# Optimization experiments

Hardware: AMD Instinct MI355X
Metric: run time of the kernel (lower is better)

Reference implementation:

```python
import jax, jax.numpy as jnp
import numpy as np

DIM_MODEL = 1024
DIM_LLM = 4096
HEAD_NUM = 16
DIM_KEYS = DIM_MODEL // HEAD_NUM  # 64


def setup_inputs() -> dict:
    key = jax.random.key(0)
    ks = jax.random.split(key, 11)
    B, P, V = 8, 256, 8192
    s_q = 1.0 / np.sqrt(DIM_MODEL)
    s_l = 1.0 / np.sqrt(DIM_LLM)
    s_d = 1.0 / np.sqrt(DIM_MODEL)
    return {
        "query": jax.random.normal(ks[0], (B, P, DIM_MODEL), dtype=jnp.float32),
        "key": jax.random.normal(ks[1], (V, DIM_LLM), dtype=jnp.float32),
        "value": jax.random.normal(ks[2], (V, DIM_LLM), dtype=jnp.float32),
        "Wq": jax.random.normal(ks[3], (DIM_MODEL, DIM_MODEL), dtype=jnp.float32) * s_q,
        "bq": jnp.zeros((DIM_MODEL,), dtype=jnp.float32),
        "Wk": jax.random.normal(ks[4], (DIM_LLM, DIM_MODEL), dtype=jnp.float32) * s_l,
        "bk": jnp.zeros((DIM_MODEL,), dtype=jnp.float32),
        "Wv": jax.random.normal(ks[5], (DIM_LLM, DIM_MODEL), dtype=jnp.float32) * s_l,
        "bv": jnp.zeros((DIM_MODEL,), dtype=jnp.float32),
        "Wo": jax.random.normal(ks[6], (DIM_MODEL, DIM_LLM), dtype=jnp.float32) * s_d,
        "bo": jnp.zeros((DIM_LLM,), dtype=jnp.float32),
    }


def reference(query, key, value, Wq, bq, Wk, bk, Wv, bv, Wo, bo):
    B, P, _ = query.shape
    V = key.shape[0]
    # projections
    q = (query @ Wq + bq).reshape(B, P, HEAD_NUM, DIM_KEYS)        # [b,p,h,k]
    k = (key @ Wk + bk).reshape(V, HEAD_NUM, DIM_KEYS)             # [v,h,k]
    v = (value @ Wv + bv).reshape(V, HEAD_NUM, DIM_KEYS)           # [v,h,k]
    scale = 1.0 / DIM_KEYS  # NOTE: original uses 1/d_k, not 1/sqrt(d_k)
    scores = jnp.einsum('bphk,vhk->bhpv', q, k)                    # [b,h,p,v]
    A = jax.nn.softmax(scale * scores, axis=-1)                    # dropout is identity in eval
    mapped = jnp.einsum('bhpv,vhk->bphk', A, v)                    # [b,p,h,k]
    mapped = mapped.reshape(B, P, HEAD_NUM * DIM_KEYS)
    return mapped @ Wo + bo                                        # [b,p,dim_llm]
```

## Files before the change

kernel.cpp:

```cpp
#include <hip/hip_runtime.h>


typedef __attribute__((ext_vector_type(8)))  short          short8;
typedef __attribute__((ext_vector_type(4)))  float          f32x4;
typedef __attribute__((ext_vector_type(16))) float          f32x16;
typedef __attribute__((ext_vector_type(8)))  unsigned short ushort8;
typedef __attribute__((ext_vector_type(4)))  unsigned int   uint4v;

__device__ __forceinline__ unsigned short f2bf(float f) {
    unsigned int u = __builtin_bit_cast(unsigned int, f);
    u += 0x7fffu + ((u >> 16) & 1u);
    return (unsigned short)(u >> 16);
}

__device__ __forceinline__ void gld_lds16(const ushort* g, ushort* l) {
    __builtin_amdgcn_global_load_lds(
        (const __attribute__((address_space(1))) void*)g,
        (__attribute__((address_space(3))) void*)l, 16, 0, 0);
}

__global__ __launch_bounds__(256) void conv_f32_bf16(
    const float* __restrict__ in, ushort* __restrict__ out, int n)
{
    int i = (blockIdx.x * 256 + threadIdx.x) * 8;
    if (i >= n) return;
    float4 a = *(const float4*)(in + i);
    float4 b = *(const float4*)(in + i + 4);
    ushort8 o = {f2bf(a.x), f2bf(a.y), f2bf(a.z), f2bf(a.w),
                 f2bf(b.x), f2bf(b.y), f2bf(b.z), f2bf(b.w)};
    *(ushort8*)(out + i) = o;
}

__global__ __launch_bounds__(256) void transconv(
    const float* __restrict__ in, ushort* __restrict__ out, int R, int C)
{
    __shared__ float t[32][33];
    const int tx = threadIdx.x & 31, ty = threadIdx.x >> 5;
    const int bx = blockIdx.x, by = blockIdx.y;
#pragma unroll
    for (int i = 0; i < 4; ++i)
        t[ty + 8 * i][tx] = in[(size_t)(by * 32 + ty + 8 * i) * C + bx * 32 + tx];
    __syncthreads();
#pragma unroll
    for (int i = 0; i < 4; ++i)
        out[(size_t)(bx * 32 + ty + 8 * i) * R + by * 32 + tx] = f2bf(t[tx][ty + 8 * i]);
}

template<int OUT_BF16, int BIAS_ROW>
__global__ __launch_bounds__(256, 4) void gemm_bt(
    const ushort* __restrict__ A, const ushort* __restrict__ BT,
    const float* __restrict__ bias, void* __restrict__ Cout,
    int M, int N, int K, float oscale)
{
    __shared__ ushort As[128 * 32];
    __shared__ ushort Bs[64 * 32];
    const int tid = threadIdx.x;
    const int w = tid >> 6, lane = tid & 63;
    const int m = lane & 15, quad = lane >> 4;
    const int wr = w >> 1, wc = w & 1;
    const int bx = blockIdx.x, by = blockIdx.y;

    f32x4 acc[4][2];
#pragma unroll
    for (int i = 0; i < 4; ++i)
#pragma unroll
        for (int j = 0; j < 2; ++j)
#pragma unroll
            for (int r = 0; r < 4; ++r) acc[i][j][r] = 0.f;

    const int r_i = lane >> 2;
    const int ccl = (lane & 3) ^ ((lane >> 2) & 3) ^ quad;
    const ushort* Ag = A  + (size_t)(by * 128 + w * 32 + r_i) * K + ccl * 8;
    const ushort* Bg = BT + (size_t)(bx * 64 + w * 16 + r_i) * K + ccl * 8;
    ushort* AsW = As + w * 1024;
    ushort* BsW = Bs + w * 512;
    const size_t rowstep = (size_t)16 * K;

    const int phys = (quad ^ (m & 3) ^ (m >> 2)) * 8;
    int aoff[4], boff[2];
#pragma unroll
    for (int i = 0; i < 4; ++i)
        aoff[i] = (wr * 64 + i * 16 + m) * 32 + phys;
#pragma unroll
    for (int j = 0; j < 2; ++j)
        boff[j] = (wc * 32 + j * 16 + m) * 32 + phys;

    const int kIters = K >> 5;
    for (int kt = 0; kt < kIters; ++kt) {
        __syncthreads();
        gld_lds16(Ag, AsW);
        gld_lds16(Ag + rowstep, AsW + 512);
        gld_lds16(Bg, BsW);
        Ag += 32; Bg += 32;
        __syncthreads();
        short8 af[4], bf[2];
#pragma unroll
        for (int i = 0; i < 4; ++i) af[i] = *(const short8*)(As + aoff[i]);
#pragma unroll
        for (int j = 0; j < 2; ++j) bf[j] = *(const short8*)(Bs + boff[j]);
#pragma unroll
        for (int i = 0; i < 4; ++i)
#pragma unroll
            for (int j = 0; j < 2; ++j)
                acc[i][j] = __builtin_amdgcn_mfma_f32_16x16x32_bf16(
                    af[i], bf[j], acc[i][j], 0, 0, 0);
    }

    const int row0 = by * 128 + wr * 64;
    const int col0 = bx * 64 + wc * 32;
#pragma unroll
    for (int i = 0; i < 4; ++i) {
#pragma unroll
        for (int j = 0; j < 2; ++j) {
            const int c = col0 + j * 16 + m;
            float bcol = BIAS_ROW ? 0.f : bias[c];
#pragma unroll
            for (int r = 0; r < 4; ++r) {
                const int rw = row0 + i * 16 + quad * 4 + r;
                float v = acc[i][j][r] + (BIAS_ROW ? bias[rw] : bcol);
                v *= oscale;
                if (OUT_BF16)
                    ((ushort*)Cout)[(size_t)rw * N + c] = f2bf(v);
                else
                    ((float*)Cout)[(size_t)rw * N + c] = v;
            }
        }
    }
}

__global__ __launch_bounds__(512, 4) void attn_mfma(
    const ushort* __restrict__ qb, const ushort* __restrict__ kb,
    const ushort* __restrict__ vT, ushort* __restrict__ mappedb)
{
    __shared__ ushort Qs[64 * 64];
    __shared__ ushort Ks[2][128 * 64];
    __shared__ ushort Vs[2][64 * 128];

    const int tid = threadIdx.x;
    const int w = tid >> 6, lane = tid & 63;
    const int l31 = lane & 31, l5 = lane >> 5, quad = lane >> 4;
    const int wp = w >> 2, wv = w & 3;
    const int idx = blockIdx.x;
    const int pt = idx & 3, h = (idx >> 2) & 15, b = idx >> 6;
    const int pbase = b * 256 + pt * 64;

    const int c8 = lane & 7, r8 = lane >> 3, c16 = lane & 15;
    const int ccK = c8 ^ r8;

    const int t0 = w * 2, t1 = w * 2 + 1;
    const ushort* gk0 = kb + (size_t)(t0 * 8 + r8) * 1024 + h * 64 + ccK * 8;
    const ushort* gk1 = kb + (size_t)(t1 * 8 + r8) * 1024 + h * 64 + ccK * 8;
    const int d0 = t0 * 4 + quad, d1 = t1 * 4 + quad;
    const ushort* gv0 = vT + (size_t)(h * 64 + d0) * 8192 + ((c16 ^ (d0 & 15)) * 8);
    const ushort* gv1 = vT + (size_t)(h * 64 + d1) * 8192 + ((c16 ^ (d1 & 15)) * 8);

    {
        const ushort* g = qb + (size_t)(pbase + w * 8 + r8) * 1024 + h * 64 + c8 * 8;
        gld_lds16(g, Qs + w * 512);
    }
    gld_lds16(gk0, Ks[0] + t0 * 512);
    gld_lds16(gk1, Ks[0] + t1 * 512);
    gld_lds16(gv0, Vs[0] + t0 * 512);
    gld_lds16(gv1, Vs[0] + t1 * 512);
    asm volatile("s_waitcnt vmcnt(4)" ::: "memory");
    __builtin_amdgcn_s_barrier();
    __builtin_amdgcn_sched_barrier(0);
    short8 qf[4];
#pragma unroll
    for (int ks = 0; ks < 4; ++ks)
        qf[ks] = *(const short8*)(Qs + (wp * 32 + l31) * 64 + ks * 16 + l5 * 8);

    f32x16 o[2];
#pragma unroll
    for (int dt = 0; dt < 2; ++dt)
#pragma unroll
        for (int r = 0; r < 16; ++r) o[dt][r] = 0.f;
    float lpart = 0.f;

    for (int t = 0; t < 64; ++t) {
        const int cur = t & 1;
        {
            const size_t koff = (size_t)(((t + 1) & 63) * 128) * 1024;
            const size_t voff = (size_t)(((t + 1) & 63) * 128);
            ushort* KsN = Ks[cur ^ 1];
            ushort* VsN = Vs[cur ^ 1];
            gld_lds16(gk0 + koff, KsN + t0 * 512);
            gld_lds16(gk1 + koff, KsN + t1 * 512);
            gld_lds16(gv0 + voff, VsN + t0 * 512);
            gld_lds16(gv1 + voff, VsN + t1 * 512);
        }
        asm volatile("s_waitcnt vmcnt(4)" ::: "memory");
        __builtin_amdgcn_s_barrier();
        __builtin_amdgcn_sched_barrier(0);

        const ushort* KsC = Ks[cur];
        const ushort* VsC = Vs[cur];

        f32x16 st;
#pragma unroll
        for (int r = 0; r < 16; ++r) st[r] = 0.f;
        {
            const int row = (wv * 32 + l31) * 64;
            const int sw = l31 & 7;
            __builtin_amdgcn_s_setprio(1);
#pragma unroll
            for (int ks = 0; ks < 4; ++ks) {
                const int ph = ((ks * 2 + l5) ^ sw) * 8;
                short8 kf = *(const short8*)(KsC + row + ph);
                st = __builtin_amdgcn_mfma_f32_32x32x16_bf16(kf, qf[ks], st, 0, 0, 0);
            }
            __builtin_amdgcn_s_setprio(0);
        }

#pragma unroll
        for (int k4 = 0; k4 < 2; ++k4) {
            float e[8];
#pragma unroll
            for (int tt = 0; tt < 8; ++tt)
                e[tt] = __builtin_amdgcn_exp2f(st[k4 * 8 + tt]);
            lpart += ((e[0] + e[1]) + (e[2] + e[3])) + ((e[4] + e[5]) + (e[6] + e[7]));
            unsigned int a0, a1, b0, b1;
            asm("v_cvt_pk_bf16_f32 %0, %1, %2" : "=v"(a0) : "v"(e[0]), "v"(e[1]));
            asm("v_cvt_pk_bf16_f32 %0, %1, %2" : "=v"(a1) : "v"(e[2]), "v"(e[3]));
            asm("v_cvt_pk_bf16_f32 %0, %1, %2" : "=v"(b0) : "v"(e[4]), "v"(e[5]));
            asm("v_cvt_pk_bf16_f32 %0, %1, %2" : "=v"(b1) : "v"(e[6]), "v"(e[7]));
            asm("v_permlane32_swap_b32 %0, %1" : "+v"(a0), "+v"(b0));
            asm("v_permlane32_swap_b32 %0, %1" : "+v"(a1), "+v"(b1));
            uint4v pfw = {a0, a1, b0, b1};
            short8 pf = __builtin_bit_cast(short8, pfw);
            const int k8 = wv * 2 + k4;
            __builtin_amdgcn_s_setprio(1);
#pragma unroll
            for (int dt = 0; dt < 2; ++dt) {
                const int d_l = dt * 32 + l31;
                const int ph = ((k8 * 2 + l5) ^ (d_l & 15)) * 8;
                short8 vf = *(const short8*)(VsC + d_l * 128 + ph);
                o[dt] = __builtin_amdgcn_mfma_f32_32x32x16_bf16(pf, vf, o[dt], 0, 0, 0);
            }
            __builtin_amdgcn_s_setprio(0);
        }
        __builtin_amdgcn_sched_barrier(0);
        __builtin_amdgcn_s_barrier();
    }

    float* RedA = (float*)Ks[0];
    float* RedB = (float*)Vs[0];
    float* Lq   = (float*)Qs;
    Lq[w * 64 + lane] = lpart;
    __syncthreads();
    if (wv >= 2) {
        float* R = (wv == 2) ? RedA : RedB;
#pragma unroll
        for (int dt = 0; dt < 2; ++dt)
#pragma unroll
            for (int r = 0; r < 16; ++r)
                R[wp * 2048 + (dt * 16 + r) * 64 + lane] = o[dt][r];
    }
    __syncthreads();
    if (wv < 2) {
        float* R = (wv == 0) ? RedA : RedB;
#pragma unroll
        for (int dt = 0; dt < 2; ++dt)
#pragma unroll
            for (int r = 0; r < 16; ++r)
                o[dt][r] += R[wp * 2048 + (dt * 16 + r) * 64 + lane];
    }
    __syncthreads();
    if (wv == 1) {
#pragma unroll
        for (int dt = 0; dt < 2; ++dt)
#pragma unroll
            for (int r = 0; r < 16; ++r)
                RedA[wp * 2048 + (dt * 16 + r) * 64 + lane] = o[dt][r];
    }
    __syncthreads();
    if (wv == 0) {
#pragma unroll
        for (int dt = 0; dt < 2; ++dt)
#pragma unroll
            for (int r = 0; r < 16; ++r)
                o[dt][r] += RedA[wp * 2048 + (dt * 16 + r) * 64 + lane];
        float lsum = (Lq[(wp * 4 + 0) * 64 + lane] + Lq[(wp * 4 + 1) * 64 + lane])
                   + (Lq[(wp * 4 + 2) * 64 + lane] + Lq[(wp * 4 + 3) * 64 + lane]);

        float lfull = lsum + __shfl_xor(lsum, 32, 64);
        float rinv = 1.0f / lfull;
#pragma unroll
        for (int r = 0; r < 16; ++r) {
            const int poff = (r & 3) + 8 * (r >> 2) + 4 * l5;
            const float sc = __shfl(rinv, poff, 64);
            const size_t grow = (size_t)(pbase + wp * 32 + poff) * 1024;
#pragma unroll
            for (int dt = 0; dt < 2; ++dt)
                mappedb[grow + h * 64 + dt * 32 + l31] = f2bf(o[dt][r] * sc);
        }
    }
}

extern "C" void kernel_launch(void* const* d_in, const int* in_sizes, int n_in,
                              void* d_out, int out_size, void* d_ws, size_t ws_size,
                              hipStream_t stream)
{
    const float* query = (const float*)d_in[0];
    const float* key   = (const float*)d_in[1];
    const float* value = (const float*)d_in[2];
    const float* Wq    = (const float*)d_in[3];
    const float* bq    = (const float*)d_in[4];
    const float* Wk    = (const float*)d_in[5];
    const float* bk    = (const float*)d_in[6];
    const float* Wv    = (const float*)d_in[7];
    const float* bv    = (const float*)d_in[8];
    const float* Wo    = (const float*)d_in[9];
    const float* bo    = (const float*)d_in[10];
    float* out = (float*)d_out;

    char* ws = (char*)d_ws;
    ushort* tmpb    = (ushort*)ws;
    ushort* wslot   = (ushort*)(ws + (64ull << 20));
    ushort* queryb  = (ushort*)(ws + (72ull << 20));
    ushort* qb      = (ushort*)(ws + (76ull << 20));
    ushort* mappedb = (ushort*)ws;
    ushort* kb      = (ushort*)d_out;
    ushort* vT      = (ushort*)((char*)d_out + (16ull << 20));

    const float QSCALE = 1.4426950408889634f / 64.0f;

    conv_f32_bf16<<<16384, 256, 0, stream>>>(key, tmpb, 8192 * 4096);
    transconv<<<dim3(32, 128), 256, 0, stream>>>(Wk, wslot, 4096, 1024);
    gemm_bt<1, 0><<<dim3(16, 64), 256, 0, stream>>>(tmpb, wslot, bk, kb,
                                                    8192, 1024, 4096, 1.0f);
    conv_f32_bf16<<<16384, 256, 0, stream>>>(value, tmpb, 8192 * 4096);
    transconv<<<dim3(32, 128), 256, 0, stream>>>(Wv, wslot, 4096, 1024);
    gemm_bt<1, 1><<<dim3(128, 8), 256, 0, stream>>>(wslot, tmpb, bv, vT,
                                                    1024, 8192, 4096, 1.0f);
    conv_f32_bf16<<<1024, 256, 0, stream>>>(query, queryb, 2048 * 1024);
    transconv<<<dim3(32, 32), 256, 0, stream>>>(Wq, wslot, 1024, 1024);
    gemm_bt<1, 0><<<dim3(16, 16), 256, 0, stream>>>(queryb, wslot, bq, qb,
                                                    2048, 1024, 1024, QSCALE);
    attn_mfma<<<512, 512, 0, stream>>>(qb, kb, vT, mappedb);
    transconv<<<dim3(128, 32), 256, 0, stream>>>(Wo, wslot, 1024, 4096);
    gemm_bt<0, 0><<<dim3(64, 16), 256, 0, stream>>>(mappedb, wslot, bo, out,
                                                    2048, 4096, 1024, 1.0f);
}
```

Baseline: 691.9 us.

## Double-buffer LDS tiles with K=64 stages in bf16 GEMM

The bf16 MFMA GEMM now uses two LDS buffers with a K-tile of 64 instead of one buffer with K=32. The next tile is prefetched via global_load_lds while MFMAs run on the current tile, and the per-iteration barrier count drops from two to one. The XOR swizzle is reworked for 64-element rows. This raises LDS use to 48KB per block and lowers the occupancy hint from 4 to 3 blocks. The last iteration issues a redundant wraparound prefetch, and the mask `& (nk-1)` is only valid when nk is a power of two.

```diff
diff --git a/kernel.cpp b/kernel.cpp
--- a/kernel.cpp
+++ b/kernel.cpp
@@ -47,13 +47,13 @@
 }
 
 template<int OUT_BF16, int BIAS_ROW>
-__global__ __launch_bounds__(256, 4) void gemm_bt(
+__global__ __launch_bounds__(256, 3) void gemm_bt(
     const ushort* __restrict__ A, const ushort* __restrict__ BT,
     const float* __restrict__ bias, void* __restrict__ Cout,
     int M, int N, int K, float oscale)
 {
-    __shared__ ushort As[128 * 32];
-    __shared__ ushort Bs[64 * 32];
+    __shared__ ushort As[2][128 * 64];
+    __shared__ ushort Bs[2][64 * 64];
     const int tid = threadIdx.x;
     const int w = tid >> 6, lane = tid & 63;
     const int m = lane & 15, quad = lane >> 4;
@@ -68,42 +68,66 @@
 #pragma unroll
             for (int r = 0; r < 4; ++r) acc[i][j][r] = 0.f;
 
-    const int r_i = lane >> 2;
-    const int ccl = (lane & 3) ^ ((lane >> 2) & 3) ^ quad;
-    const ushort* Ag = A  + (size_t)(by * 128 + w * 32 + r_i) * K + ccl * 8;
-    const ushort* Bg = BT + (size_t)(bx * 64 + w * 16 + r_i) * K + ccl * 8;
-    ushort* AsW = As + w * 1024;
-    ushort* BsW = Bs + w * 512;
-    const size_t rowstep = (size_t)16 * K;
-
-    const int phys = (quad ^ (m & 3) ^ (m >> 2)) * 8;
-    int aoff[4], boff[2];
-#pragma unroll
-    for (int i = 0; i < 4; ++i)
-        aoff[i] = (wr * 64 + i * 16 + m) * 32 + phys;
-#pragma unroll
-    for (int j = 0; j < 2; ++j)
-        boff[j] = (wc * 32 + j * 16 + m) * 32 + phys;
-
-    const int kIters = K >> 5;
-    for (int kt = 0; kt < kIters; ++kt) {
-        __syncthreads();
-        gld_lds16(Ag, AsW);
-        gld_lds16(Ag + rowstep, AsW + 512);
-        gld_lds16(Bg, BsW);
-        Ag += 32; Bg += 32;
-        __syncthreads();
-        short8 af[4], bf[2];
-#pragma unroll
-        for (int i = 0; i < 4; ++i) af[i] = *(const short8*)(As + aoff[i]);
-#pragma unroll
-        for (int j = 0; j < 2; ++j) bf[j] = *(const short8*)(Bs + boff[j]);
+    const int l8 = lane >> 3, c8l = lane & 7;
+    const int ccl = c8l ^ l8;
+    const ushort* Ag = A  + (size_t)(by * 128 + w * 32 + l8) * K + ccl * 8;
+    const ushort* Bg = BT + (size_t)(bx * 64 + w * 16 + l8) * K + ccl * 8;
+    const size_t row8 = (size_t)8 * K;
+
+    auto STAGE = [&](int buf, int kt2) {
+        const ushort* a = Ag + (size_t)kt2 * 64;
+        const ushort* b = Bg + (size_t)kt2 * 64;
+        ushort* as = &As[buf][w * 2048];
+        ushort* bs = &Bs[buf][w * 1024];
+        gld_lds16(a,            as);
+        gld_lds16(a + row8,     as + 512);
+        gld_lds16(a + 2 * row8, as + 1024);
+        gld_lds16(a + 3 * row8, as + 1536);
+        gld_lds16(b,            bs);
+        gld_lds16(b + row8,     bs + 512);
+    };
+
+    int aoff[2][4], boff[2][2];
+#pragma unroll
+    for (int ks = 0; ks < 2; ++ks) {
+        const int ch = ((ks * 4 + quad) ^ (m & 7)) * 8;
 #pragma unroll
         for (int i = 0; i < 4; ++i)
-#pragma unroll
-            for (int j = 0; j < 2; ++j)
-                acc[i][j] = __builtin_amdgcn_mfma_f32_16x16x32_bf16(
-                    af[i], bf[j], acc[i][j], 0, 0, 0);
+            aoff[ks][i] = (wr * 64 + i * 16 + m) * 64 + ch;
+#pragma unroll
+        for (int j = 0; j < 2; ++j)
+            boff[ks][j] = (wc * 32 + j * 16 + m) * 64 + ch;
+    }
+
+    const int nk = K >> 6;
+    STAGE(0, 0);
+    asm volatile("s_waitcnt vmcnt(0)" ::: "memory");
+    __builtin_amdgcn_s_barrier();
+    __builtin_amdgcn_sched_barrier(0);
+
+    for (int kt = 0; kt < nk; ++kt) {
+        const int cur = kt & 1;
+        STAGE(cur ^ 1, (kt + 1) & (nk - 1));
+
+        const ushort* Asc = As[cur];
+        const ushort* Bsc = Bs[cur];
+#pragma unroll
+        for (int ks = 0; ks < 2; ++ks) {
+            short8 af[4], bfr[2];
+#pragma unroll
+            for (int i = 0; i < 4; ++i) af[i] = *(const short8*)(Asc + aoff[ks][i]);
+#pragma unroll
+            for (int j = 0; j < 2; ++j) bfr[j] = *(const short8*)(Bsc + boff[ks][j]);
+#pragma unroll
+            for (int i = 0; i < 4; ++i)
+#pragma unroll
+                for (int j = 0; j < 2; ++j)
+                    acc[i][j] = __builtin_amdgcn_mfma_f32_16x16x32_bf16(
+                        af[i], bfr[j], acc[i][j], 0, 0, 0);
+        }
+        asm volatile("s_waitcnt vmcnt(0)" ::: "memory");
+        __builtin_amdgcn_s_barrier();
+        __builtin_amdgcn_sched_barrier(0);
     }
 
     const int row0 = by * 128 + wr * 64;
```

New measurement: 780.4 us. 12.8% more time.
